# Kernel tuning notes

Hardware: AMD Instinct MI355X
Metric: run time of the kernel (lower is better)

Reference implementation:

```python
import jax, jax.numpy as jnp
import numpy as np

SIZES = (32, 64, 128, 256, 512)
RATIOS = (0.5, 1.0, 2.0)
STRIDE = 4
H = W = 256
IMG = 1024.0
NMS_THRESH = 0.7
MIN_SIZE = 1.0
BBOX_XFORM_CLIP = float(np.log(1000.0 / 16.0))
NEG = -1e9


def _make_anchors():
    # generate_anchors: ratio-major, scale-minor ordering, centered, rounded
    scales = np.asarray(SIZES, np.float32)
    ratios = np.asarray(RATIOS, np.float32)
    h_r = np.sqrt(ratios)
    w_r = 1.0 / h_r
    ws = (w_r[:, None] * scales[None, :]).reshape(-1)
    hs = (h_r[:, None] * scales[None, :]).reshape(-1)
    base = np.round(np.stack([-ws, -hs, ws, hs], axis=1) / 2.0)  # [A,4]
    # grid_anchors: (y,x)-major shifts, anchors innermost
    sx = np.arange(W, dtype=np.float32) * STRIDE
    sy = np.arange(H, dtype=np.float32) * STRIDE
    yy, xx = np.meshgrid(sy, sx, indexing="ij")
    shifts = np.stack([xx.ravel(), yy.ravel(), xx.ravel(), yy.ravel()], 1)  # [H*W,4]
    return (shifts[:, None, :] + base[None, :, :]).reshape(-1, 4).astype(np.float32)


def setup_inputs() -> dict:
    key = jax.random.key(0)
    k1, k2 = jax.random.split(key)
    N, A = 8, len(SIZES) * len(RATIOS)
    objectness = jax.random.normal(k1, (N, A, H, W), jnp.float32)
    box_regression = jax.random.normal(k2, (N, A * 4, H, W), jnp.float32) * 0.5
    anchors = jnp.asarray(_make_anchors())  # [H*W*A, 4]
    return {"objectness": objectness, "box_regression": box_regression,
            "anchors": anchors, "pre_nms_top_n": 2000}


def _decode(deltas, anchors):
    # BoxCoder.decode_single with weights (1,1,1,1)
    w = anchors[:, 2] - anchors[:, 0]
    h = anchors[:, 3] - anchors[:, 1]
    cx = anchors[:, 0] + 0.5 * w
    cy = anchors[:, 1] + 0.5 * h
    dx, dy = deltas[:, 0], deltas[:, 1]
    dw = jnp.minimum(deltas[:, 2], BBOX_XFORM_CLIP)
    dh = jnp.minimum(deltas[:, 3], BBOX_XFORM_CLIP)
    pcx = dx * w + cx
    pcy = dy * h + cy
    pw = jnp.exp(dw) * w
    ph = jnp.exp(dh) * h
    return jnp.stack([pcx - 0.5 * pw, pcy - 0.5 * ph,
                      pcx + 0.5 * pw, pcy + 0.5 * ph], axis=1)


def _nms_keep(boxes, thresh):
    # boxes [K,4] sorted by descending score; greedy NMS via fixed fori_loop
    x1, y1, x2, y2 = boxes[:, 0], boxes[:, 1], boxes[:, 2], boxes[:, 3]
    area = (x2 - x1) * (y2 - y1)
    lt = jnp.maximum(boxes[:, None, :2], boxes[None, :, :2])
    rb = jnp.minimum(boxes[:, None, 2:], boxes[None, :, 2:])
    wh = jnp.clip(rb - lt, 0.0)
    inter = wh[..., 0] * wh[..., 1]
    iou = inter / (area[:, None] + area[None, :] - inter)
    K = boxes.shape[0]
    rng = jnp.arange(K)

    def body(i, keep):
        sup = keep[i] & (iou[i] > thresh) & (rng > i)
        return keep & ~sup

    return jax.lax.fori_loop(0, K, body, jnp.ones((K,), bool))


def reference(objectness, box_regression, anchors, pre_nms_top_n):
    N, A, Hf, Wf = objectness.shape
    # permute_and_flatten: [N,A,H,W] -> [N, H*W*A] (h,w-major, anchor-minor)
    scores = objectness.transpose(0, 2, 3, 1).reshape(N, -1)
    deltas = (box_regression.reshape(N, A, 4, Hf, Wf)
              .transpose(0, 3, 4, 1, 2).reshape(N, -1, 4))
    proposals = jax.vmap(lambda d: _decode(d, anchors))(deltas)  # [N,M,4]
    # clip_boxes_to_image
    bx = jnp.clip(proposals[..., 0::2], 0.0, IMG)
    by = jnp.clip(proposals[..., 1::2], 0.0, IMG)
    proposals = jnp.stack([bx[..., 0], by[..., 0], bx[..., 1], by[..., 1]], -1)
    probs = jax.nn.sigmoid(scores)
    # remove_small_boxes (mask with -inf score instead of dynamic filter)
    valid = ((proposals[..., 2] - proposals[..., 0]) >= MIN_SIZE) & \
            ((proposals[..., 3] - proposals[..., 1]) >= MIN_SIZE)
    probs = jnp.where(valid, probs, NEG)
    top_scores, top_idx = jax.lax.top_k(probs, pre_nms_top_n)  # [N,K]
    top_boxes = jnp.take_along_axis(proposals, top_idx[..., None], axis=1)
    keep = jax.vmap(lambda b: _nms_keep(b, NMS_THRESH))(top_boxes)  # [N,K] bool
    kf = keep.astype(top_boxes.dtype)
    return jnp.concatenate([top_boxes * kf[..., None],
                            (top_scores * kf)[..., None]], axis=-1)  # [N,K,5]
```

## Files before the change

### kernel.cpp

```cpp
#include <hip/hip_runtime.h>
#include <stdint.h>

#define N_    8
#define A_    15
#define H_    256
#define W_    256
#define M_    (A_*H_*W_)
#define BINS  8192
#define BSH   19
#define KMAJ  3200
#define CAP   8192
#define CBUF  2048
#define WPR   32

__device__ __constant__ double CLIP_  = 4.135166556742356;
__device__ __constant__ double IMG_   = 1024.0;
__device__ __constant__ double MINSZ_ = 1.0;
__device__ __constant__ double NMST_  = 0.7;

__device__ __forceinline__ uint32_t ord32(float s) {
    uint32_t u = __float_as_uint(s);
    return u ^ (uint32_t)(((int32_t)u >> 31) | 0x80000000u);
}

__device__ __forceinline__ void decode_box(
    const float* __restrict__ breg, const float* __restrict__ anchors,
    int n, int a, int hw, int m,
    double& x1, double& y1, double& x2, double& y2)
{
    size_t bbase = ((size_t)(n*60 + a*4)) * 65536 + (size_t)hw;
    double d0 = (double)breg[bbase];
    double d1 = (double)breg[bbase + 65536];
    double d2 = (double)breg[bbase + 2*65536];
    double d3 = (double)breg[bbase + 3*65536];
    float4 av = *reinterpret_cast<const float4*>(anchors + (size_t)m*4);
    double a0 = (double)av.x, a1 = (double)av.y, a2 = (double)av.z, a3 = (double)av.w;
    double ww = a2 - a0, hh = a3 - a1;
    double cx = a0 + 0.5*ww, cy = a1 + 0.5*hh;
    double dw = fmin(d2, CLIP_), dh = fmin(d3, CLIP_);
    double pcx = d0*ww + cx, pcy = d1*hh + cy;
    double pw = exp(dw)*ww, ph = exp(dh)*hh;
    x1 = pcx - 0.5*pw; y1 = pcy - 0.5*ph;
    x2 = pcx + 0.5*pw; y2 = pcy + 0.5*ph;
    x1 = fmin(fmax(x1, 0.0), IMG_);
    y1 = fmin(fmax(y1, 0.0), IMG_);
    x2 = fmin(fmax(x2, 0.0), IMG_);
    y2 = fmin(fmax(y2, 0.0), IMG_);
}

__global__ void k_zero(uint4* __restrict__ p, int n16)
{
    int i = blockIdx.x*blockDim.x + threadIdx.x;
    if (i < n16) p[i] = make_uint4(0u, 0u, 0u, 0u);
}

__global__ void k_hist(const float* __restrict__ obj, unsigned int* __restrict__ hist)
{
    __shared__ unsigned int lh[BINS];
    const int n = blockIdx.y;
    for (int i = threadIdx.x; i < BINS; i += blockDim.x) lh[i] = 0;
    __syncthreads();
    const float4* objq = (const float4*)(obj + (size_t)n * M_);
    for (int it = 0; it < 32; ++it) {
        int q = blockIdx.x * 8192 + it * 256 + threadIdx.x;
        float4 v = objq[q];
        atomicAdd(&lh[ord32(v.x) >> BSH], 1u);
        atomicAdd(&lh[ord32(v.y) >> BSH], 1u);
        atomicAdd(&lh[ord32(v.z) >> BSH], 1u);
        atomicAdd(&lh[ord32(v.w) >> BSH], 1u);
    }
    __syncthreads();
    for (int i = threadIdx.x; i < BINS; i += blockDim.x) {
        unsigned int c = lh[i];
        if (c) atomicAdd(&hist[n*BINS + i], c);
    }
}

__global__ void k_findT(const unsigned int* __restrict__ hist, unsigned int* __restrict__ T)
{
    __shared__ unsigned int csum[256];
    const int n = blockIdx.x;
    const int tid = threadIdx.x;
    unsigned int s = 0;
    int hi = BINS - 1 - tid*32;
    for (int i = 0; i < 32; ++i) s += hist[n*BINS + hi - i];
    csum[tid] = s;
    __syncthreads();
    if (tid == 0) {
        unsigned int cum = 0; int c = 0;
        for (; c < 256; ++c) { if (cum + csum[c] >= (unsigned)KMAJ) break; cum += csum[c]; }
        if (c == 256) { T[n] = 0; return; }
        int hi2 = BINS - 1 - c*32;
        unsigned int cum2 = cum; int b = hi2;
        for (int i = 0; i < 32; ++i) {
            b = hi2 - i;
            cum2 += hist[n*BINS + b];
            if (cum2 >= (unsigned)KMAJ) break;
        }
        if (cum2 > (unsigned)CAP && b < BINS-1) b = b + 1;
        T[n] = (unsigned int)b;
    }
}

__global__ void k_collect(const float* __restrict__ obj, const float* __restrict__ breg,
                          const float* __restrict__ anchors, const unsigned int* __restrict__ T,
                          unsigned int* __restrict__ cnt, uint64_t* __restrict__ cand)
{
    __shared__ uint64_t buf[CBUF];
    __shared__ unsigned int lcnt, gbase;
    const int n = blockIdx.y;
    const unsigned int Tn = T[n];
    if (threadIdx.x == 0) lcnt = 0;
    __syncthreads();
    const float4* objq = (const float4*)(obj + (size_t)n * M_);
    for (int it = 0; it < 32; ++it) {
        int q = blockIdx.x * 8192 + it * 256 + threadIdx.x;
        float4 v = objq[q];
        int a = q >> 14;
        int hwq = q & 16383;
        #pragma unroll
        for (int e = 0; e < 4; ++e) {
            float s = (e==0) ? v.x : (e==1) ? v.y : (e==2) ? v.z : v.w;
            unsigned int o = ord32(s);
            if ((o >> BSH) < Tn) continue;
            int hw = hwq*4 + e;
            int m = hw*15 + a;
            double x1,y1,x2,y2;
            decode_box(breg, anchors, n, a, hw, m, x1,y1,x2,y2);
            if (!((x2 - x1 >= MINSZ_) && (y2 - y1 >= MINSZ_))) continue;
            uint64_t key = ((uint64_t)o << 32) | (uint32_t)(~(uint32_t)m);
            unsigned int p = atomicAdd(&lcnt, 1u);
            if (p < CBUF) buf[p] = key;
            else {
                unsigned int g = atomicAdd(&cnt[n*32], 1u);
                if (g < CAP) cand[(size_t)n*CAP + g] = key;
            }
        }
    }
    __syncthreads();
    if (threadIdx.x == 0) {
        unsigned int c = min(lcnt, (unsigned int)CBUF);
        gbase = atomicAdd(&cnt[n*32], c);
    }
    __syncthreads();
    unsigned int c = min(lcnt, (unsigned int)CBUF);
    for (unsigned int i = threadIdx.x; i < c; i += 256) {
        unsigned int g = gbase + i;
        if (g < CAP) cand[(size_t)n*CAP + g] = buf[i];
    }
}

__global__ void k_sort1k(uint64_t* __restrict__ cand, const unsigned int* __restrict__ cnt)
{
    __shared__ uint64_t s[1024];
    const int n = blockIdx.y, c = blockIdx.x;
    unsigned int cn = cnt[n*32]; if (cn > CAP) cn = CAP;
    uint64_t* base = cand + (size_t)n*CAP + c*1024;
    const int rem = (int)cn - c*1024;
    for (int i = threadIdx.x; i < 1024; i += blockDim.x)
        s[i] = (i < rem) ? base[i] : 0ull;
    __syncthreads();
    for (int k = 2; k <= 1024; k <<= 1) {
        for (int j = k >> 1; j > 0; j >>= 1) {
            for (int i = threadIdx.x; i < 1024; i += blockDim.x) {
                int l = i ^ j;
                if (l > i) {
                    uint64_t A = s[i], B = s[l];
                    bool up = ((i & k) == 0);
                    if ((A < B) == up) { s[i] = B; s[l] = A; }
                }
            }
            __syncthreads();
        }
    }
    for (int i = threadIdx.x; i < 1024; i += blockDim.x)
        base[i] = s[i];
}

__global__ void k_merge1(const uint64_t* __restrict__ cand, uint64_t* __restrict__ runs1)
{
    __shared__ uint64_t s[2048];
    const int n = blockIdx.y, jb = blockIdx.x;
    const uint64_t* A = cand + (size_t)n*CAP + (2*jb)*1024;
    const uint64_t* B = cand + (size_t)n*CAP + (2*jb+1)*1024;
    for (int i = threadIdx.x; i < 1024; i += blockDim.x) {
        uint64_t a = A[i], b = B[1023 - i];
        s[i]        = (a > b) ? a : b;
        s[i + 1024] = (a > b) ? b : a;
    }
    __syncthreads();
    for (int j = 512; j > 0; j >>= 1) {
        for (int i = threadIdx.x; i < 2048; i += blockDim.x) {
            int l = i ^ j;
            if (l > i) {
                uint64_t A2 = s[i], B2 = s[l];
                if (A2 < B2) { s[i] = B2; s[l] = A2; }
            }
        }
        __syncthreads();
    }
    uint64_t* dst = runs1 + ((size_t)n*4 + jb)*2048;
    for (int i = threadIdx.x; i < 2048; i += blockDim.x)
        dst[i] = s[i];
}

__device__ __forceinline__ void trunc_merge_body(
    const uint64_t* __restrict__ A, const uint64_t* __restrict__ B, uint64_t* s)
{
    for (int i = threadIdx.x; i < 2048; i += blockDim.x) {
        uint64_t a = A[i], b = B[2047 - i];
        s[i] = (a > b) ? a : b;
    }
    __syncthreads();
    for (int j = 1024; j > 0; j >>= 1) {
        for (int i = threadIdx.x; i < 2048; i += blockDim.x) {
            int l = i ^ j;
            if (l > i) {
                uint64_t A2 = s[i], B2 = s[l];
                if (A2 < B2) { s[i] = B2; s[l] = A2; }
            }
        }
        __syncthreads();
    }
}

__global__ void k_merge2(const uint64_t* __restrict__ runs1, uint64_t* __restrict__ runs2)
{
    __shared__ uint64_t s[2048];
    const int n = blockIdx.y, jb = blockIdx.x;
    trunc_merge_body(runs1 + ((size_t)n*4 + 2*jb)*2048,
                     runs1 + ((size_t)n*4 + 2*jb + 1)*2048, s);
    uint64_t* dst = runs2 + ((size_t)n*2 + jb)*2048;
    for (int i = threadIdx.x; i < 2048; i += blockDim.x)
        dst[i] = s[i];
}

__global__ void k_merge3_decode(const uint64_t* __restrict__ runs2,
                                const float* __restrict__ obj,
                                const float* __restrict__ breg,
                                const float* __restrict__ anchors,
                                double* __restrict__ boxes, double* __restrict__ probs,
                                int K)
{
    __shared__ uint64_t s[2048];
    const int n = blockIdx.x;
    trunc_merge_body(runs2 + ((size_t)n*2)*2048,
                     runs2 + ((size_t)n*2 + 1)*2048, s);
    for (int i = threadIdx.x; i < K; i += blockDim.x) {
        unsigned int m = ~((uint32_t)s[i]);
        int t = n*K + i;
        if (m >= (unsigned int)M_) {
            boxes[(size_t)t*4+0]=0.0; boxes[(size_t)t*4+1]=0.0;
            boxes[(size_t)t*4+2]=0.0; boxes[(size_t)t*4+3]=0.0;
            probs[t] = -1000000000.0;
            continue;
        }
        int a = (int)(m % 15u);
        int hw = (int)(m / 15u);
        double x1,y1,x2,y2;
        decode_box(breg, anchors, n, a, hw, (int)m, x1,y1,x2,y2);
        double* bx = boxes + (size_t)t*4;
        bx[0]=x1; bx[1]=y1; bx[2]=x2; bx[3]=y2;
        float sc = obj[((size_t)(n*15 + a)) * 65536 + hw];
        probs[t] = 1.0 / (1.0 + exp(-(double)sc));
    }
}

__global__ void k_sup(const double* __restrict__ boxes, uint64_t* __restrict__ sup, int K)
{
    __shared__ double jb[128][5];
    const int n = blockIdx.y;
    const int ntiles = (K + 127) >> 7;
    int p = blockIdx.x, ti = 0, rem = ntiles;
    while (p >= rem) { p -= rem; ++ti; --rem; }
    const int tj = ti + p;

    const int rowsj = min(128, K - tj*128);
    for (int x = threadIdx.x; x < rowsj*4; x += 256)
        jb[x >> 2][x & 3] = boxes[(((size_t)n*K) + tj*128)*4 + x];
    __syncthreads();
    if (threadIdx.x < (unsigned)rowsj)
        jb[threadIdx.x][4] = (jb[threadIdx.x][2]-jb[threadIdx.x][0]) *
                             (jb[threadIdx.x][3]-jb[threadIdx.x][1]);
    __syncthreads();

    const int il = threadIdx.x >> 1;
    const int word = threadIdx.x & 1;
    const int i = ti*128 + il;
    if (i >= K) return;

    const double* bi = boxes + (((size_t)n*K) + i)*4;
    double ix1=bi[0], iy1=bi[1], ix2=bi[2], iy2=bi[3];
    double ai = (ix2-ix1)*(iy2-iy1);

    uint64_t bits = 0;
    const int jb0 = word*64;
    const int jlim = min(rowsj - jb0, 64);
    const int jg0 = tj*128 + jb0;
    for (int b = 0; b < jlim; ++b) {
        int j = jg0 + b;
        if (j <= i) continue;
        double jx1=jb[jb0+b][0], jy1=jb[jb0+b][1], jx2=jb[jb0+b][2], jy2=jb[jb0+b][3];
        double aj = jb[jb0+b][4];
        double lx = fmax(ix1, jx1), ly = fmax(iy1, jy1);
        double rx = fmin(ix2, jx2), ry = fmin(iy2, jy2);
        double wx = fmax(rx - lx, 0.0), wy = fmax(ry - ly, 0.0);
        double inter = wx * wy;
        double iou = inter / (ai + aj - inter);
        if (iou > NMST_) bits |= (1ull << b);
    }
    sup[(((size_t)n*K) + i)*WPR + (tj*2 + word)] = bits;
}

#define RL_(r) (((uint64_t)(uint32_t)__builtin_amdgcn_readlane(dhi,(r)) << 32) \
              |  (uint64_t)(uint32_t)__builtin_amdgcn_readlane(dlo,(r)))
#define ST_(r, rw) { uint64_t msk_ = (uint64_t)0 - ((alive >> (r)) & 1ull); \
                     alive &= ~((rw) & msk_); }
__global__ void __launch_bounds__(256) k_nms_out(
    const uint64_t* __restrict__ sup, const double* __restrict__ boxes,
    const double* __restrict__ probs, float* __restrict__ out, int K)
{
    __shared__ uint64_t buf[2][64][WPR+1];
    __shared__ uint64_t keep_lds[WPR];
    const int n = blockIdx.x;
    const int tid = threadIdx.x;
    const int nch = (K + 63) >> 6;

    uint64_t keepw = 0;
    if (tid < WPR) {
        int base = tid * 64;
        if (base + 64 <= K) keepw = ~0ull;
        else if (base < K)  keepw = (~0ull) >> (64 - (K - base));
    }

    {
        const int tot = min(64, K) * WPR;
        const uint64_t* src = sup + ((size_t)n*K)*WPR;
        uint64_t tmp[8];
        #pragma unroll
        for (int k = 0; k < 8; ++k) {
            int x = tid + 256*k;
            tmp[k] = (x < tot) ? src[x] : 0ull;
        }
        #pragma unroll
        for (int k = 0; k < 8; ++k) {
            int x = tid + 256*k;
            if (x < tot) buf[0][x >> 5][x & 31] = tmp[k];
        }
    }
    __syncthreads();

    for (int c = 0; c < nch; ++c) {
        const int cur = c & 1;
        if (tid >= 64 && c + 1 < nch) {
            const int c1 = c + 1;
            const int i0 = c1 * 64;
            const int rows = min(64, K - i0);
            const uint64_t* src = sup + (((size_t)n*K) + i0)*WPR;
            const int t = tid - 64;
            const int lane_w = t & 31;
            const int rg = t >> 5;
            const int w = c1 + lane_w;
            uint64_t tmp[11];
            #pragma unroll
            for (int k = 0; k < 11; ++k) {
                int row = rg + 6*k;
                bool p = (w < WPR) && (row < rows);
                tmp[k] = p ? src[(size_t)row*WPR + w] : 0ull;
            }
            #pragma unroll
            for (int k = 0; k < 11; ++k) {
                int row = rg + 6*k;
                if ((w < WPR) && (row < rows)) buf[cur ^ 1][row][w] = tmp[k];
            }
        }
        if (tid < 64) {
            uint64_t diag = buf[cur][tid][c];
            uint32_t dlo = (uint32_t)diag;
            uint32_t dhi = (uint32_t)(diag >> 32);
            uint32_t alo = (uint32_t)__builtin_amdgcn_readlane((uint32_t)keepw, c);
            uint32_t ahi = (uint32_t)__builtin_amdgcn_readlane((uint32_t)(keepw >> 32), c);
            uint64_t alive = ((uint64_t)ahi << 32) | (uint64_t)alo;
            #pragma unroll
            for (int b = 0; b < 8; ++b) {
                const int r0b = b * 8;
                uint64_t w0_ = RL_(r0b + 0);
                uint64_t w1_ = RL_(r0b + 1);
                uint64_t w2_ = RL_(r0b + 2);
                uint64_t w3_ = RL_(r0b + 3);
                uint64_t w4_ = RL_(r0b + 4);
                uint64_t w5_ = RL_(r0b + 5);
                uint64_t w6_ = RL_(r0b + 6);
                uint64_t w7_ = RL_(r0b + 7);
                ST_(r0b + 0, w0_);
                ST_(r0b + 1, w1_);
                ST_(r0b + 2, w2_);
                ST_(r0b + 3, w3_);
                ST_(r0b + 4, w4_);
                ST_(r0b + 5, w5_);
                ST_(r0b + 6, w6_);
                ST_(r0b + 7, w7_);
            }
            if (tid == c) keepw = alive;
            const int w = tid & 31;
            const int r0 = (tid >> 5) * 32;
            uint64_t pend = 0;
            #pragma unroll
            for (int rr = 0; rr < 32; ++rr) {
                int r = r0 + rr;
                uint64_t msk = (uint64_t)0 - ((alive >> r) & 1ull);
                pend |= buf[cur][r][w] & msk;
            }
            pend |= (uint64_t)__shfl_xor((unsigned long long)pend, 32, 64);
            if (tid < WPR && tid > c) keepw &= ~pend;
        }
        __syncthreads();
    }

    if (tid < WPR) keep_lds[tid] = keepw;
    __syncthreads();

    for (int k = tid; k < K; k += 256) {
        uint64_t w = keep_lds[k >> 6];
        double f = ((w >> (k & 63)) & 1ull) ? 1.0 : 0.0;
        const double* b = boxes + (((size_t)n*K) + k)*4;
        float* o = out + (((size_t)n*K) + k)*5;
        o[0] = (float)(b[0]*f);
        o[1] = (float)(b[1]*f);
        o[2] = (float)(b[2]*f);
        o[3] = (float)(b[3]*f);
        o[4] = (float)(probs[(size_t)n*K + k]*f);
    }
}

extern "C" void kernel_launch(void* const* d_in, const int* in_sizes, int n_in,
                              void* d_out, int out_size, void* d_ws, size_t ws_size,
                              hipStream_t stream)
{
    const float* obj     = (const float*)d_in[0];
    const float* breg    = (const float*)d_in[1];
    const float* anchors = (const float*)d_in[2];
    float* out = (float*)d_out;

    const int K = out_size / (N_ * 5);

    char* ws = (char*)d_ws;
    unsigned int* hist  = (unsigned int*)(ws + 0);
    unsigned int* T     = (unsigned int*)(ws + 262144);
    unsigned int* cnt   = (unsigned int*)(ws + 262272);
    double*       boxes = (double*)      (ws + 327680);
    double*       probs = (double*)      (ws + 839680);
    uint64_t*     sup   = (uint64_t*)    (ws + 970752);
    uint64_t*     cand  = (uint64_t*)    (ws + 970752);
    uint64_t*     runs1 = (uint64_t*)    (ws + 970752 + 524288);
    uint64_t*     runs2 = (uint64_t*)    (ws + 970752 + 1048576);

    const int n16 = 263296 / 16;
    k_zero<<<(n16 + 255)/256, 256, 0, stream>>>((uint4*)ws, n16);

    dim3 gH(30, N_);
    k_hist<<<gH, 256, 0, stream>>>(obj, hist);
    k_findT<<<N_, 256, 0, stream>>>(hist, T);
    k_collect<<<gH, 256, 0, stream>>>(obj, breg, anchors, T, cnt, cand);
    k_sort1k<<<dim3(8, N_), 512, 0, stream>>>(cand, cnt);
    k_merge1<<<dim3(4, N_), 1024, 0, stream>>>(cand, runs1);
    k_merge2<<<dim3(2, N_), 1024, 0, stream>>>(runs1, runs2);
    k_merge3_decode<<<N_, 1024, 0, stream>>>(runs2, obj, breg, anchors, boxes, probs, K);
    const int ntiles = (K + 127) >> 7;
    dim3 gS(ntiles*(ntiles+1)/2, N_);
    k_sup<<<gS, 256, 0, stream>>>(boxes, sup, K);
    k_nms_out<<<N_, 256, 0, stream>>>(sup, boxes, probs, out, K);
}
```

Measured before the change: 228.7 us.

## Fuse threshold search into collect and merge stages into one kernel

Moves the per-image threshold search into each k_collect block, so every block recomputes it from the histogram instead of a separate k_findT launch writing T. The three merge kernels are folded into one 1024-thread block per image that keeps all 8192 candidates in 64KB of LDS and does the three merge levels there, dropping the runs1/runs2 global round trips and three launches. The trade-off is redundant threshold work in all 240 collect blocks and only 8 blocks doing the whole merge, which lowers parallelism in that stage.

```diff
diff --git a/kernel.cpp b/kernel.cpp
--- a/kernel.cpp
+++ b/kernel.cpp
@@ -76,42 +76,40 @@
     }
 }
 
-__global__ void k_findT(const unsigned int* __restrict__ hist, unsigned int* __restrict__ T)
-{
+__global__ void k_collect(const float* __restrict__ obj, const float* __restrict__ breg,
+                          const float* __restrict__ anchors, const unsigned int* __restrict__ hist,
+                          unsigned int* __restrict__ cnt, uint64_t* __restrict__ cand)
+{
+    __shared__ uint64_t buf[CBUF];
     __shared__ unsigned int csum[256];
-    const int n = blockIdx.x;
-    const int tid = threadIdx.x;
-    unsigned int s = 0;
-    int hi = BINS - 1 - tid*32;
-    for (int i = 0; i < 32; ++i) s += hist[n*BINS + hi - i];
-    csum[tid] = s;
-    __syncthreads();
-    if (tid == 0) {
-        unsigned int cum = 0; int c = 0;
-        for (; c < 256; ++c) { if (cum + csum[c] >= (unsigned)KMAJ) break; cum += csum[c]; }
-        if (c == 256) { T[n] = 0; return; }
-        int hi2 = BINS - 1 - c*32;
-        unsigned int cum2 = cum; int b = hi2;
-        for (int i = 0; i < 32; ++i) {
-            b = hi2 - i;
-            cum2 += hist[n*BINS + b];
-            if (cum2 >= (unsigned)KMAJ) break;
-        }
-        if (cum2 > (unsigned)CAP && b < BINS-1) b = b + 1;
-        T[n] = (unsigned int)b;
-    }
-}
-
-__global__ void k_collect(const float* __restrict__ obj, const float* __restrict__ breg,
-                          const float* __restrict__ anchors, const unsigned int* __restrict__ T,
-                          unsigned int* __restrict__ cnt, uint64_t* __restrict__ cand)
-{
-    __shared__ uint64_t buf[CBUF];
-    __shared__ unsigned int lcnt, gbase;
+    __shared__ unsigned int lcnt, gbase, Tn_s;
     const int n = blockIdx.y;
-    const unsigned int Tn = T[n];
-    if (threadIdx.x == 0) lcnt = 0;
-    __syncthreads();
+    {
+        unsigned int sss = 0;
+        int hi = BINS - 1 - threadIdx.x*32;
+        for (int i2 = 0; i2 < 32; ++i2) sss += hist[n*BINS + hi - i2];
+        csum[threadIdx.x] = sss;
+        if (threadIdx.x == 0) lcnt = 0;
+        __syncthreads();
+        if (threadIdx.x == 0) {
+            unsigned int cum = 0; int c = 0;
+            for (; c < 256; ++c) { if (cum + csum[c] >= (unsigned)KMAJ) break; cum += csum[c]; }
+            if (c == 256) { Tn_s = 0; }
+            else {
+                int hi2 = BINS - 1 - c*32;
+                unsigned int cum2 = cum; int b = hi2;
+                for (int i2 = 0; i2 < 32; ++i2) {
+                    b = hi2 - i2;
+                    cum2 += hist[n*BINS + b];
+                    if (cum2 >= (unsigned)KMAJ) break;
+                }
+                if (cum2 > (unsigned)CAP && b < BINS-1) b = b + 1;
+                Tn_s = (unsigned int)b;
+            }
+        }
+        __syncthreads();
+    }
+    const unsigned int Tn = Tn_s;
     const float4* objq = (const float4*)(obj + (size_t)n * M_);
     for (int it = 0; it < 32; ++it) {
         int q = blockIdx.x * 8192 + it * 256 + threadIdx.x;
@@ -177,20 +175,28 @@
         base[i] = s[i];
 }
 
-__global__ void k_merge1(const uint64_t* __restrict__ cand, uint64_t* __restrict__ runs1)
-{
-    __shared__ uint64_t s[2048];
-    const int n = blockIdx.y, jb = blockIdx.x;
-    const uint64_t* A = cand + (size_t)n*CAP + (2*jb)*1024;
-    const uint64_t* B = cand + (size_t)n*CAP + (2*jb+1)*1024;
-    for (int i = threadIdx.x; i < 1024; i += blockDim.x) {
-        uint64_t a = A[i], b = B[1023 - i];
-        s[i]        = (a > b) ? a : b;
-        s[i + 1024] = (a > b) ? b : a;
+__global__ void k_mergeall(const uint64_t* __restrict__ cand,
+                           const float* __restrict__ obj,
+                           const float* __restrict__ breg,
+                           const float* __restrict__ anchors,
+                           double* __restrict__ boxes, double* __restrict__ probs,
+                           int K)
+{
+    __shared__ uint64_t s[8192];
+    const int n = blockIdx.x;
+    const int tid = threadIdx.x;
+    const uint64_t* base = cand + (size_t)n*CAP;
+
+    #pragma unroll
+    for (int p = 0; p < 4; ++p) {
+        uint64_t a = base[(2*p)*1024 + tid];
+        uint64_t b = base[(2*p+1)*1024 + 1023 - tid];
+        s[p*2048 + tid]        = (a > b) ? a : b;
+        s[p*2048 + 1024 + tid] = (a > b) ? b : a;
     }
     __syncthreads();
     for (int j = 512; j > 0; j >>= 1) {
-        for (int i = threadIdx.x; i < 2048; i += blockDim.x) {
+        for (int i = tid; i < 8192; i += 1024) {
             int l = i ^ j;
             if (l > i) {
                 uint64_t A2 = s[i], B2 = s[l];
@@ -199,21 +205,23 @@
         }
         __syncthreads();
     }
-    uint64_t* dst = runs1 + ((size_t)n*4 + jb)*2048;
-    for (int i = threadIdx.x; i < 2048; i += blockDim.x)
-        dst[i] = s[i];
-}
-
-__device__ __forceinline__ void trunc_merge_body(
-    const uint64_t* __restrict__ A, const uint64_t* __restrict__ B, uint64_t* s)
-{
-    for (int i = threadIdx.x; i < 2048; i += blockDim.x) {
-        uint64_t a = A[i], b = B[2047 - i];
-        s[i] = (a > b) ? a : b;
+
+    {
+        uint64_t q0a = s[tid],        t0;
+        t0 = s[2048 + 2047 - tid]; if (t0 > q0a) q0a = t0;
+        uint64_t q0b = s[tid + 1024];
+        t0 = s[2048 + 1023 - tid]; if (t0 > q0b) q0b = t0;
+        uint64_t q1a = s[4096 + tid];
+        t0 = s[6144 + 2047 - tid]; if (t0 > q1a) q1a = t0;
+        uint64_t q1b = s[4096 + tid + 1024];
+        t0 = s[6144 + 1023 - tid]; if (t0 > q1b) q1b = t0;
+        __syncthreads();
+        s[tid] = q0a; s[tid + 1024] = q0b;
+        s[2048 + tid] = q1a; s[2048 + tid + 1024] = q1b;
     }
     __syncthreads();
     for (int j = 1024; j > 0; j >>= 1) {
-        for (int i = threadIdx.x; i < 2048; i += blockDim.x) {
+        for (int i = tid; i < 4096; i += 1024) {
             int l = i ^ j;
             if (l > i) {
                 uint64_t A2 = s[i], B2 = s[l];
@@ -222,31 +230,28 @@
         }
         __syncthreads();
     }
-}
-
-__global__ void k_merge2(const uint64_t* __restrict__ runs1, uint64_t* __restrict__ runs2)
-{
-    __shared__ uint64_t s[2048];
-    const int n = blockIdx.y, jb = blockIdx.x;
-    trunc_merge_body(runs1 + ((size_t)n*4 + 2*jb)*2048,
-                     runs1 + ((size_t)n*4 + 2*jb + 1)*2048, s);
-    uint64_t* dst = runs2 + ((size_t)n*2 + jb)*2048;
-    for (int i = threadIdx.x; i < 2048; i += blockDim.x)
-        dst[i] = s[i];
-}
-
-__global__ void k_merge3_decode(const uint64_t* __restrict__ runs2,
-                                const float* __restrict__ obj,
-                                const float* __restrict__ breg,
-                                const float* __restrict__ anchors,
-                                double* __restrict__ boxes, double* __restrict__ probs,
-                                int K)
-{
-    __shared__ uint64_t s[2048];
-    const int n = blockIdx.x;
-    trunc_merge_body(runs2 + ((size_t)n*2)*2048,
-                     runs2 + ((size_t)n*2 + 1)*2048, s);
-    for (int i = threadIdx.x; i < K; i += blockDim.x) {
+
+    {
+        uint64_t m0 = s[tid], t0;
+        t0 = s[2048 + 2047 - tid]; if (t0 > m0) m0 = t0;
+        uint64_t m1 = s[tid + 1024];
+        t0 = s[2048 + 1023 - tid]; if (t0 > m1) m1 = t0;
+        __syncthreads();
+        s[tid] = m0; s[tid + 1024] = m1;
+    }
+    __syncthreads();
+    for (int j = 1024; j > 0; j >>= 1) {
+        for (int i = tid; i < 2048; i += 1024) {
+            int l = i ^ j;
+            if (l > i) {
+                uint64_t A2 = s[i], B2 = s[l];
+                if (A2 < B2) { s[i] = B2; s[l] = A2; }
+            }
+        }
+        __syncthreads();
+    }
+
+    for (int i = tid; i < K; i += 1024) {
         unsigned int m = ~((uint32_t)s[i]);
         int t = n*K + i;
         if (m >= (unsigned int)M_) {
@@ -446,26 +451,20 @@
 
     char* ws = (char*)d_ws;
     unsigned int* hist  = (unsigned int*)(ws + 0);
-    unsigned int* T     = (unsigned int*)(ws + 262144);
     unsigned int* cnt   = (unsigned int*)(ws + 262272);
     double*       boxes = (double*)      (ws + 327680);
     double*       probs = (double*)      (ws + 839680);
     uint64_t*     sup   = (uint64_t*)    (ws + 970752);
     uint64_t*     cand  = (uint64_t*)    (ws + 970752);
-    uint64_t*     runs1 = (uint64_t*)    (ws + 970752 + 524288);
-    uint64_t*     runs2 = (uint64_t*)    (ws + 970752 + 1048576);
 
     const int n16 = 263296 / 16;
     k_zero<<<(n16 + 255)/256, 256, 0, stream>>>((uint4*)ws, n16);
 
     dim3 gH(30, N_);
     k_hist<<<gH, 256, 0, stream>>>(obj, hist);
-    k_findT<<<N_, 256, 0, stream>>>(hist, T);
-    k_collect<<<gH, 256, 0, stream>>>(obj, breg, anchors, T, cnt, cand);
+    k_collect<<<gH, 256, 0, stream>>>(obj, breg, anchors, hist, cnt, cand);
     k_sort1k<<<dim3(8, N_), 512, 0, stream>>>(cand, cnt);
-    k_merge1<<<dim3(4, N_), 1024, 0, stream>>>(cand, runs1);
-    k_merge2<<<dim3(2, N_), 1024, 0, stream>>>(runs1, runs2);
-    k_merge3_decode<<<N_, 1024, 0, stream>>>(runs2, obj, breg, anchors, boxes, probs, K);
+    k_mergeall<<<N_, 1024, 0, stream>>>(cand, obj, breg, anchors, boxes, probs, K);
     const int ntiles = (K + 127) >> 7;
     dim3 gS(ntiles*(ntiles+1)/2, N_);
     k_sup<<<gS, 256, 0, stream>>>(boxes, sup, K);
```

Result: no change. 231.5 us (+1.2%).
